# Performance work log

Hardware: AMD Instinct MI355X
Metric: run time of the kernel (lower is better)

The kernel has to match this reference:

```python
import jax, jax.numpy as jnp
import numpy as np

N = 100000  # number of events; must be a multiple of 10 in the original code


def setup_inputs() -> dict:
    key = jax.random.key(0)
    ks = jax.random.split(key, 9)
    x = jax.random.normal(ks[0], (N, 20, 4, 3), dtype=jnp.float32)
    # stand-in LorentzNN scoring head: flattened (4,3)=12 features -> 2 logits
    Wl = jax.random.normal(ks[1], (12, 2), dtype=jnp.float32) * 0.3
    bl = jnp.zeros((2,), dtype=jnp.float32)
    # MLP weights, kaiming fan_in init as in torch
    W1 = jax.random.normal(ks[2], (80, 20), dtype=jnp.float32) * np.sqrt(2.0 / 20)
    b1 = jnp.zeros((80,), dtype=jnp.float32)
    W2 = jax.random.normal(ks[3], (40, 80), dtype=jnp.float32) * np.sqrt(2.0 / 80)
    b2 = jnp.zeros((40,), dtype=jnp.float32)
    W3 = jax.random.normal(ks[4], (21, 40), dtype=jnp.float32) * np.sqrt(2.0 / 40)
    b3 = jnp.zeros((21,), dtype=jnp.float32)
    return {"x": x, "Wl": Wl, "bl": bl, "W1": W1, "b1": b1,
            "W2": W2, "b2": b2, "W3": W3, "b3": b3}


def reference(x, Wl, bl, W1, b1, W2, b2, W3, b3):
    # x: [N, 20, 4, 3] -> per-triplet features [N, 20, 12]
    feats = x.reshape(x.shape[0], 20, 12)
    # LorentzNN stand-in: 2 logits per triplet, take logit index 1 (score[1])
    logits = jnp.einsum("ntf,fc->ntc", feats, Wl) + bl  # [N, 20, 2]
    s = logits[..., 1]                                   # [N, 20]
    # 3-layer MLP 20 -> 80 -> 40 -> 21
    h = jax.nn.relu(s @ W1.T + b1)
    h = jax.nn.relu(h @ W2.T + b2)
    out = h @ W3.T + b3                                  # [N, 21]
    return out
```

## Files before the change

### kernel.cpp

```cpp
#include <hip/hip_runtime.h>

typedef _Float16 f16;
typedef _Float16 f16x8 __attribute__((ext_vector_type(8)));
typedef float    f32x4 __attribute__((ext_vector_type(4)));

#define WF1_OFF 0
#define WF2_OFF 2560
#define WF3_OFF 7168
#define WF_TOTAL 9216
#define WAVES 4
#define H_STRIDE 3072

__global__ void prep_kernel(const float* __restrict__ W1, const float* __restrict__ b1,
                            const float* __restrict__ W2, const float* __restrict__ b2,
                            const float* __restrict__ W3, const float* __restrict__ b3,
                            f16* __restrict__ wf) {
    const int t0 = blockIdx.x * blockDim.x + threadIdx.x;
    const int stride = gridDim.x * blockDim.x;
    for (int idx = t0; idx < 5 * 512; idx += stride) {
        int j = idx & 7, l = (idx >> 3) & 63, nt = idx >> 9;
        int nn = nt * 16 + (l & 15);
        int k  = (l >> 4) * 8 + j;
        float v = (k < 20) ? W1[nn * 20 + k] : (k == 20 ? b1[nn] : 0.f);
        wf[WF1_OFF + idx] = (f16)v;
    }
    for (int idx = t0; idx < 9 * 512; idx += stride) {
        int j = idx & 7, l = (idx >> 3) & 63, grp = idx >> 9;
        int nt = grp % 3, ks = grp / 3;
        int nn = nt * 16 + (l & 15);
        int k  = ks * 32 + (l >> 4) * 8 + j;
        float v = 0.f;
        if (nn < 40) { if (k < 80) v = W2[nn * 80 + k]; else if (k == 80) v = b2[nn]; }
        wf[WF2_OFF + idx] = (f16)v;
    }
    for (int idx = t0; idx < 4 * 512; idx += stride) {
        int j = idx & 7, l = (idx >> 3) & 63, grp = idx >> 9;
        int nt = grp & 1, ks = grp >> 1;
        int nn = nt * 16 + (l & 15);
        int k  = ks * 32 + (l >> 4) * 8 + j;
        float v = 0.f;
        if (nn < 21) { if (k < 40) v = W3[nn * 40 + k]; else if (k == 40) v = b3[nn]; }
        wf[WF3_OFF + idx] = (f16)v;
    }
}

__global__ __launch_bounds__(256, 8) void fused_kernel(
    const float* __restrict__ x,
    const float* __restrict__ Wl,
    const float* __restrict__ bl,
    const f16*   __restrict__ wf,
    float* __restrict__ out,
    int n)
{
    __shared__ __align__(16) f16 s_lds[64][40];
    __shared__ __align__(16) char hbuf[WAVES * H_STRIDE];

    const int tid  = threadIdx.x;
    const int wave = tid >> 6;
    const int lane = tid & 63;
    const int lrow = lane & 15;
    const int lg   = lane >> 4;

    char* hb = hbuf + wave * H_STRIDE;

    {
        int* z1 = reinterpret_cast<int*>(hb + 2560);
        z1[lane] = 0; z1[lane + 64] = 0;
        if (lane < 16) *reinterpret_cast<f16*>(hb + (10 * 16 + lane) * 16) = (f16)1.f;
    }

#pragma unroll
    for (int it = 0; it < 3; ++it) {
        int idx = it * 256 + tid;
        int row = idx / 12, c = idx % 12;
        s_lds[row][20 + c] = (c == 0) ? (f16)1.f : (f16)0.f;
    }

    float wl[12];
#pragma unroll
    for (int f = 0; f < 12; ++f) wl[f] = Wl[f * 2 + 1];
    const float blv = bl[1];

    const int n_trip = n * 20;
    const int trip_base = blockIdx.x * 1280;
#pragma unroll
    for (int r = 0; r < 5; ++r) {
        const int bt = r * 256 + tid;
        const int trip = trip_base + bt;
        if (trip < n_trip) {
            const float4* xt = reinterpret_cast<const float4*>(x + (size_t)trip * 12);
            float4 a0 = xt[0], a1 = xt[1], a2 = xt[2];
            float acc = blv;
            acc += a0.x*wl[0] + a0.y*wl[1] + a0.z*wl[2]  + a0.w*wl[3];
            acc += a1.x*wl[4] + a1.y*wl[5] + a1.z*wl[6]  + a1.w*wl[7];
            acc += a2.x*wl[8] + a2.y*wl[9] + a2.z*wl[10] + a2.w*wl[11];
            s_lds[bt / 20][bt % 20] = (f16)acc;
        }
    }

    __syncthreads();

    const int ev0 = blockIdx.x * (WAVES * 16) + wave * 16;
    if (ev0 >= n) return;

    const f16x8* bfrag = reinterpret_cast<const f16x8*>(wf);
    const f32x4 zero4 = {0.f, 0.f, 0.f, 0.f};

    f16x8 a1 = *reinterpret_cast<const f16x8*>(&s_lds[wave * 16 + lrow][lg * 8]);
    f32x4 acc1[5];
#pragma unroll
    for (int nt = 0; nt < 5; ++nt)
        acc1[nt] = __builtin_amdgcn_mfma_f32_16x16x32_f16(
            a1, bfrag[(WF1_OFF / 8) + nt * 64 + lane], zero4, 0, 0, 0);
#pragma unroll
    for (int nt = 0; nt < 5; ++nt) {
        const int neuron = nt * 16 + lrow;
#pragma unroll
        for (int r = 0; r < 4; ++r) {
            float v = fmaxf(acc1[nt][r], 0.f);
            reinterpret_cast<f16*>(hb + ((neuron >> 3) * 16 + lg * 4 + r) * 16)[neuron & 7] = (f16)v;
        }
    }

    f32x4 acc2[3] = {zero4, zero4, zero4};
#pragma unroll
    for (int ks = 0; ks < 3; ++ks) {
        f16x8 a = *reinterpret_cast<const f16x8*>(hb + ((ks * 4 + lg) * 16 + lrow) * 16);
#pragma unroll
        for (int nt = 0; nt < 3; ++nt)
            acc2[nt] = __builtin_amdgcn_mfma_f32_16x16x32_f16(
                a, bfrag[(WF2_OFF / 8) + (ks * 3 + nt) * 64 + lane], acc2[nt], 0, 0, 0);
    }

    {
        int* z2 = reinterpret_cast<int*>(hb + 1280);
        z2[lane] = 0; z2[lane + 64] = 0; z2[lane + 128] = 0;
        if (lane < 16) *reinterpret_cast<f16*>(hb + (5 * 16 + lane) * 16) = (f16)1.f;
    }
#pragma unroll
    for (int nt = 0; nt < 3; ++nt) {
        const int nn = nt * 16 + lrow;
#pragma unroll
        for (int r = 0; r < 4; ++r) {
            float v = fmaxf(acc2[nt][r], 0.f);
            if (nn < 40)
                reinterpret_cast<f16*>(hb + ((nn >> 3) * 16 + lg * 4 + r) * 16)[nn & 7] = (f16)v;
        }
    }

    f32x4 acc3[2] = {zero4, zero4};
#pragma unroll
    for (int ks = 0; ks < 2; ++ks) {
        f16x8 a = *reinterpret_cast<const f16x8*>(hb + ((ks * 4 + lg) * 16 + lrow) * 16);
#pragma unroll
        for (int nt = 0; nt < 2; ++nt)
            acc3[nt] = __builtin_amdgcn_mfma_f32_16x16x32_f16(
                a, bfrag[(WF3_OFF / 8) + (ks * 2 + nt) * 64 + lane], acc3[nt], 0, 0, 0);
    }
#pragma unroll
    for (int nt = 0; nt < 2; ++nt) {
        const int col = nt * 16 + lrow;
        if (col < 21) {
#pragma unroll
            for (int r = 0; r < 4; ++r)
                out[(size_t)(ev0 + lg * 4 + r) * 21 + col] = acc3[nt][r];
        }
    }
}

extern "C" void kernel_launch(void* const* d_in, const int* in_sizes, int n_in,
                              void* d_out, int out_size, void* d_ws, size_t ws_size,
                              hipStream_t stream) {
    const float* x  = (const float*)d_in[0];
    const float* Wl = (const float*)d_in[1];
    const float* bl = (const float*)d_in[2];
    const float* W1 = (const float*)d_in[3];
    const float* b1 = (const float*)d_in[4];
    const float* W2 = (const float*)d_in[5];
    const float* b2 = (const float*)d_in[6];
    const float* W3 = (const float*)d_in[7];
    const float* b3 = (const float*)d_in[8];
    float* out = (float*)d_out;

    const int n = in_sizes[0] / 240;
    f16* wf = (f16*)d_ws;

    prep_kernel<<<16, 256, 0, stream>>>(W1, b1, W2, b2, W3, b3, wf);

    const int grid = (n + 63) / 64;
    fused_kernel<<<grid, 256, 0, stream>>>(x, Wl, bl, wf, out, n);
}
```

Measured before the change: 29.22 us.

## Fuse weight prep into main kernel, staging swizzled fp16 weights in LDS

Drops the separate prep kernel launch. Each block now converts W1/W2/W3 and the biases into MFMA fragment layout itself and writes them to shared memory with an XOR swizzle, and the B fragments are read from LDS instead of global memory. This removes one kernel launch and its dependency, but every block redoes the weight conversion, adds about 18KB of LDS per block, and lowers the launch-bounds occupancy hint from 8 to 4.

```diff
diff --git a/kernel.cpp b/kernel.cpp
--- a/kernel.cpp
+++ b/kernel.cpp
@@ -11,47 +11,24 @@
 #define WAVES 4
 #define H_STRIDE 3072
 
-__global__ void prep_kernel(const float* __restrict__ W1, const float* __restrict__ b1,
-                            const float* __restrict__ W2, const float* __restrict__ b2,
-                            const float* __restrict__ W3, const float* __restrict__ b3,
-                            f16* __restrict__ wf) {
-    const int t0 = blockIdx.x * blockDim.x + threadIdx.x;
-    const int stride = gridDim.x * blockDim.x;
-    for (int idx = t0; idx < 5 * 512; idx += stride) {
-        int j = idx & 7, l = (idx >> 3) & 63, nt = idx >> 9;
-        int nn = nt * 16 + (l & 15);
-        int k  = (l >> 4) * 8 + j;
-        float v = (k < 20) ? W1[nn * 20 + k] : (k == 20 ? b1[nn] : 0.f);
-        wf[WF1_OFF + idx] = (f16)v;
-    }
-    for (int idx = t0; idx < 9 * 512; idx += stride) {
-        int j = idx & 7, l = (idx >> 3) & 63, grp = idx >> 9;
-        int nt = grp % 3, ks = grp / 3;
-        int nn = nt * 16 + (l & 15);
-        int k  = ks * 32 + (l >> 4) * 8 + j;
-        float v = 0.f;
-        if (nn < 40) { if (k < 80) v = W2[nn * 80 + k]; else if (k == 80) v = b2[nn]; }
-        wf[WF2_OFF + idx] = (f16)v;
-    }
-    for (int idx = t0; idx < 4 * 512; idx += stride) {
-        int j = idx & 7, l = (idx >> 3) & 63, grp = idx >> 9;
-        int nt = grp & 1, ks = grp >> 1;
-        int nn = nt * 16 + (l & 15);
-        int k  = ks * 32 + (l >> 4) * 8 + j;
-        float v = 0.f;
-        if (nn < 21) { if (k < 40) v = W3[nn * 40 + k]; else if (k == 40) v = b3[nn]; }
-        wf[WF3_OFF + idx] = (f16)v;
-    }
+__device__ __forceinline__ int swz(int h) {
+    return h ^ (((h >> 6) & 7) << 3);
 }
 
-__global__ __launch_bounds__(256, 8) void fused_kernel(
+__global__ __launch_bounds__(256, 4) void fused_kernel(
     const float* __restrict__ x,
     const float* __restrict__ Wl,
     const float* __restrict__ bl,
-    const f16*   __restrict__ wf,
+    const float* __restrict__ W1,
+    const float* __restrict__ b1,
+    const float* __restrict__ W2,
+    const float* __restrict__ b2,
+    const float* __restrict__ W3,
+    const float* __restrict__ b3,
     float* __restrict__ out,
     int n)
 {
+    __shared__ __align__(16) f16 wfl[WF_TOTAL];
     __shared__ __align__(16) f16 s_lds[64][40];
     __shared__ __align__(16) char hbuf[WAVES * H_STRIDE];
 
@@ -60,6 +37,39 @@
     const int lane = tid & 63;
     const int lrow = lane & 15;
     const int lg   = lane >> 4;
+    const int lswz = (lane & 56) | ((lane & 7) ^ ((lane >> 3) & 7));
+
+#pragma unroll
+    for (int it = 0; it < 10; ++it) {
+        int idx = it * 256 + tid;
+        int j = idx & 7, l = (idx >> 3) & 63, nt = idx >> 9;
+        int nn = nt * 16 + (l & 15);
+        int k  = (l >> 4) * 8 + j;
+        float v = (k < 20) ? W1[nn * 20 + k] : (k == 20 ? b1[nn] : 0.f);
+        wfl[swz(WF1_OFF + idx)] = (f16)v;
+    }
+#pragma unroll
+    for (int it = 0; it < 18; ++it) {
+        int idx = it * 256 + tid;
+        int j = idx & 7, l = (idx >> 3) & 63, grp = idx >> 9;
+        int nt = grp % 3, ks = grp / 3;
+        int nn = nt * 16 + (l & 15);
+        int k  = ks * 32 + (l >> 4) * 8 + j;
+        float v = 0.f;
+        if (nn < 40) { if (k < 80) v = W2[nn * 80 + k]; else if (k == 80) v = b2[nn]; }
+        wfl[swz(WF2_OFF + idx)] = (f16)v;
+    }
+#pragma unroll
+    for (int it = 0; it < 8; ++it) {
+        int idx = it * 256 + tid;
+        int j = idx & 7, l = (idx >> 3) & 63, grp = idx >> 9;
+        int nt = grp & 1, ks = grp >> 1;
+        int nn = nt * 16 + (l & 15);
+        int k  = ks * 32 + (l >> 4) * 8 + j;
+        float v = 0.f;
+        if (nn < 21) { if (k < 40) v = W3[nn * 40 + k]; else if (k == 40) v = b3[nn]; }
+        wfl[swz(WF3_OFF + idx)] = (f16)v;
+    }
 
     char* hb = hbuf + wave * H_STRIDE;
 
@@ -103,7 +113,7 @@
     const int ev0 = blockIdx.x * (WAVES * 16) + wave * 16;
     if (ev0 >= n) return;
 
-    const f16x8* bfrag = reinterpret_cast<const f16x8*>(wf);
+    const f16x8* bfrag = reinterpret_cast<const f16x8*>(wfl);
     const f32x4 zero4 = {0.f, 0.f, 0.f, 0.f};
 
     f16x8 a1 = *reinterpret_cast<const f16x8*>(&s_lds[wave * 16 + lrow][lg * 8]);
@@ -111,7 +121,7 @@
 #pragma unroll
     for (int nt = 0; nt < 5; ++nt)
         acc1[nt] = __builtin_amdgcn_mfma_f32_16x16x32_f16(
-            a1, bfrag[(WF1_OFF / 8) + nt * 64 + lane], zero4, 0, 0, 0);
+            a1, bfrag[(WF1_OFF / 8) + nt * 64 + lswz], zero4, 0, 0, 0);
 #pragma unroll
     for (int nt = 0; nt < 5; ++nt) {
         const int neuron = nt * 16 + lrow;
@@ -129,7 +139,7 @@
 #pragma unroll
         for (int nt = 0; nt < 3; ++nt)
             acc2[nt] = __builtin_amdgcn_mfma_f32_16x16x32_f16(
-                a, bfrag[(WF2_OFF / 8) + (ks * 3 + nt) * 64 + lane], acc2[nt], 0, 0, 0);
+                a, bfrag[(WF2_OFF / 8) + (ks * 3 + nt) * 64 + lswz], acc2[nt], 0, 0, 0);
     }
 
     {
@@ -155,7 +165,7 @@
 #pragma unroll
         for (int nt = 0; nt < 2; ++nt)
             acc3[nt] = __builtin_amdgcn_mfma_f32_16x16x32_f16(
-                a, bfrag[(WF3_OFF / 8) + (ks * 2 + nt) * 64 + lane], acc3[nt], 0, 0, 0);
+                a, bfrag[(WF3_OFF / 8) + (ks * 2 + nt) * 64 + lswz], acc3[nt], 0, 0, 0);
     }
 #pragma unroll
     for (int nt = 0; nt < 2; ++nt) {
@@ -183,10 +193,7 @@
     float* out = (float*)d_out;
 
     const int n = in_sizes[0] / 240;
-    f16* wf = (f16*)d_ws;
-
-    prep_kernel<<<16, 256, 0, stream>>>(W1, b1, W2, b2, W3, b3, wf);
-
     const int grid = (n + 63) / 64;
-    fused_kernel<<<grid, 256, 0, stream>>>(x, Wl, bl, wf, out, n);
+    fused_kernel<<<grid, 256, 0, stream>>>(x, Wl, bl, W1, b1, W2, b2, W3, b3,
+                                           out, n);
 }
```

Measured after the change: 36.12 us. 1.24x slower.
